# Kernel tuning notes

Hardware: AMD Instinct MI355X
Metric: run time of the kernel (lower is better)

The kernel has to match this reference:

```python
import jax, jax.numpy as jnp
import numpy as np

B, C, H, T, L = 128, 16, 9, 2048, 9  # batch, channels, sensors, time, decomp levels
TAU = 1.0

def _conv(x, w, pad):
    # x: [N,C,H,W], w: [O,I,kh,kw]
    return jax.lax.conv_general_dilated(x, w, (1, 1), pad,
                                        dimension_numbers=('NCHW', 'OIHW', 'NCHW'))

def _prelu(x, a):
    return jnp.where(x >= 0, x, a * x)

def _branch(z, w1, a, w2):
    # ReflectionPad2d((1,1,0,0)) -> Conv(1,3) -> PReLU -> Conv(1,1) -> Tanh
    z = jnp.pad(z, ((0, 0), (0, 0), (0, 0), (1, 1)), mode='reflect')
    z = _prelu(_conv(z, w1, [(0, 0), (0, 0)]), a)
    return jnp.tanh(_conv(z, w2, [(0, 0), (0, 0)]))


def setup_inputs() -> dict:
    key = jax.random.key(0)
    ks = jax.random.split(key, 24)
    n = lambda k, s, sc=0.05: jax.random.normal(k, s, dtype=jnp.float32) * sc
    u = jax.random.uniform(ks[1], (L, 2 * B, 2, 1, 1), dtype=jnp.float32,
                           minval=1e-6, maxval=1.0 - 1e-6)
    inp = {
        'x': jax.random.normal(ks[0], (B, 1, H, T), dtype=jnp.float32),
        'gumbel_noise': -jnp.log(-jnp.log(u)),
        # conv_in stem
        'Wc1': n(ks[2], (C, 1, 1, 33)), 'bc1': jnp.zeros((C,), jnp.float32),
        'bn1_g': jnp.ones((C,), jnp.float32), 'bn1_b': jnp.zeros((C,), jnp.float32),
        'a_c1': jnp.float32(0.25),
        'Wc2': n(ks[3], (C, C, 1, 3)), 'bc2': jnp.zeros((C,), jnp.float32),
        'bn2_g': jnp.ones((C,), jnp.float32), 'bn2_b': jnp.zeros((C,), jnp.float32),
        'a_c2': jnp.float32(0.25),
        # per-level lifting P/U branches
        'WP1': n(ks[4], (L, C, C, 1, 3)), 'aP': jnp.full((L,), 0.25, jnp.float32),
        'WP2': n(ks[5], (L, C, C, 1, 1)),
        'WU1': n(ks[6], (L, C, C, 1, 3)), 'aU': jnp.full((L,), 0.25, jnp.float32),
        'WU2': n(ks[7], (L, C, C, 1, 1)),
        # per-level gumble routing head (pooled -> 1x1 C->C -> PReLU -> 1x1 C->2 -> PReLU)
        'Wg1': n(ks[8], (L, C, C, 1, 1)), 'ag1': jnp.full((L,), 0.25, jnp.float32),
        'Wg2': n(ks[9], (L, 2, C, 1, 1)), 'ag2': jnp.full((L,), 0.25, jnp.float32),
    }
    return inp


def _forward(x, Wc1, bc1, bn1_g, bn1_b, a_c1, Wc2, bc2, bn2_g, bn2_b, a_c2,
             WP1, aP, WP2, WU1, aU, WU2, Wg1, ag1, Wg2, ag2, gumbel_noise):
    rs = lambda v: v.reshape(1, -1, 1, 1)
    # conv_in stem (BatchNorm in eval form with default running stats)
    x = _conv(x, Wc1, [(0, 0), (16, 16)]) + rs(bc1)
    x = _prelu(x * rs(bn1_g) + rs(bn1_b), a_c1)
    x = _conv(x, Wc2, [(0, 0), (1, 1)]) + rs(bc2)
    x = _prelu(x * rs(bn2_g) + rs(bn2_b), a_c2)  # [B,C,H,T]

    feats = []
    for i in range(L):
        even, odd = x[..., ::2], x[..., 1::2]
        # modified lifting: c = even + U(odd); d = odd - P(c)
        c = even + _branch(odd, WU1[i], aU[i], WU2[i])
        d = odd - _branch(c, WP1[i], aP[i], WP2[i])
        out = jnp.stack([c, d], axis=1)  # [B,2,C,H,t]
        t = out.shape[-1]
        # gumble_block_2D: pool each (low/high) slice to [2B,C,1,1]
        pooled = out.reshape(B * 2, C, H, t).mean(axis=(2, 3), keepdims=True)
        hm = _prelu(_conv(pooled, Wg1[i], [(0, 0), (0, 0)]), ag1[i])
        hm = _prelu(_conv(hm, Wg2[i], [(0, 0), (0, 0)]), ag2[i])  # [2B,2,1,1]
        s = jax.nn.softmax(hm, axis=1)
        m = jax.nn.softmax((s + gumbel_noise[i]) / TAU, axis=1)
        m = m.reshape(B, 2, 2, 1, 1)
        input_conv = out * m[:, :, 0][..., None]  # gated conv branch [B,2,C,H,t]
        input_res = out * m[:, :, 1][..., None]   # gated residual branch
        feats.append(input_res.mean(axis=-1))      # [B,2,C,H]
        x = input_conv[:, 0]                       # gated low-pass feeds next level
    return jnp.stack(feats, axis=-1)  # [B,2,C,H,L]


def reference(x, gumbel_noise, Wc1, bc1, bn1_g, bn1_b, a_c1, Wc2, bc2, bn2_g,
              bn2_b, a_c2, WP1, aP, WP2, WU1, aU, WU2, Wg1, ag1, Wg2, ag2):
    return _forward(x, Wc1, bc1, bn1_g, bn1_b, a_c1, Wc2, bc2, bn2_g, bn2_b,
                    a_c2, WP1, aP, WP2, WU1, aU, WU2, Wg1, ag1, Wg2, ag2,
                    gumbel_noise)
```

## Files before the change

kernel.cpp:

```cpp
#include <hip/hip_runtime.h>
#include <hip/hip_bf16.h>


#define CB 16
#define HH 9
#define TT0 2048
#define RS_SLOT 36864
#define LPITCH 20

__device__ __forceinline__ float ftanh(float x) {
    float e = __expf(2.f * x);
    return 1.f - 2.f / (e + 1.f);
}
__device__ __forceinline__ float fprelu(float v, float a) {
    return v >= 0.f ? v : a * v;
}
__device__ __forceinline__ void ld16(const float* p, float* v) {
#pragma unroll
    for (int q = 0; q < 4; ++q) {
        float4 f = *(const float4*)(p + 4 * q);
        v[4 * q] = f.x; v[4 * q + 1] = f.y; v[4 * q + 2] = f.z; v[4 * q + 3] = f.w;
    }
}
__device__ __forceinline__ void ld16s(const float* p, float* v) {
#pragma unroll
    for (int q = 0; q < 4; ++q) {
        float4 f = *(const float4*)(p + 4 * q);
        v[4 * q] = f.x; v[4 * q + 1] = f.y; v[4 * q + 2] = f.z; v[4 * q + 3] = f.w;
    }
}
__device__ __forceinline__ void st16(float* p, const float* v) {
#pragma unroll
    for (int q = 0; q < 4; ++q) {
        float4 f; f.x = v[4 * q]; f.y = v[4 * q + 1]; f.z = v[4 * q + 2]; f.w = v[4 * q + 3];
        *(float4*)(p + 4 * q) = f;
    }
}
__device__ __forceinline__ int refl(int u, int t) {
    return u < 0 ? -u : (u >= t ? 2 * t - 2 - u : u);
}

__device__ __forceinline__ void gate_eval(
    const float* __restrict__ g144, const float* __restrict__ Wg1,
    float ag1, float ag2, const float* __restrict__ Wg2,
    float inv, float gn0, float gn1, float* m0o, float* m1o)
{
    float pooled[CB];
#pragma unroll
    for (int cc = 0; cc < CB; ++cc) {
        float s = 0.f;
#pragma unroll
        for (int h = 0; h < HH; ++h) s += g144[cc * HH + h];
        pooled[cc] = s * inv;
    }
    float hm1[CB];
#pragma unroll
    for (int cc = 0; cc < CB; ++cc) {
        float s = 0.f;
#pragma unroll
        for (int c2 = 0; c2 < CB; ++c2) s = fmaf(Wg1[cc * CB + c2], pooled[c2], s);
        hm1[cc] = fprelu(s, ag1);
    }
    float h0 = 0.f, h1 = 0.f;
#pragma unroll
    for (int c2 = 0; c2 < CB; ++c2) {
        h0 = fmaf(Wg2[c2], hm1[c2], h0);
        h1 = fmaf(Wg2[CB + c2], hm1[c2], h1);
    }
    h0 = fprelu(h0, ag2); h1 = fprelu(h1, ag2);
    float mx = fmaxf(h0, h1);
    float e0 = __expf(h0 - mx), e1 = __expf(h1 - mx);
    float s0 = e0 / (e0 + e1), s1 = e1 / (e0 + e1);
    float a0 = s0 + gn0, a1 = s1 + gn1;
    float mx2 = fmaxf(a0, a1);
    float f0 = __expf(a0 - mx2), f1 = __expf(a1 - mx2);
    *m0o = f0 / (f0 + f1);
    *m1o = f1 / (f0 + f1);
}

__device__ __forceinline__ void rowsum_reduce(const float* vals, float* rs, int tile,
                                              int b, int h, int sdx, int tid) {
    __shared__ float red[4 * CB];
    const int lane = tid & 63, wv = tid >> 6;
    __syncthreads();
#pragma unroll
    for (int cc = 0; cc < CB; ++cc) {
        float s = vals[cc];
#pragma unroll
        for (int off = 32; off >= 1; off >>= 1) s += __shfl_xor(s, off, 64);
        if (lane == cc) red[wv * CB + cc] = s;
    }
    __syncthreads();
    if (tid < CB) {
        float s = red[tid] + red[CB + tid] + red[2 * CB + tid] + red[3 * CB + tid];
        rs[(size_t)tile * RS_SLOT + ((size_t)(2 * b + sdx) * CB + tid) * HH + h] = s;
    }
    __syncthreads();
}

__global__ void wtrans_kernel(const float* __restrict__ Wc1, const float* __restrict__ Wc2,
                              const float* __restrict__ WU1, const float* __restrict__ WU2,
                              const float* __restrict__ WP1, const float* __restrict__ WP2,
                              float* __restrict__ W)
{
    const int tid = threadIdx.x;
    for (int idx = tid; idx < 528; idx += 256) {
        int k = idx >> 4, cc = idx & 15;
        W[idx] = Wc1[cc * 33 + k];
    }
    for (int idx = tid; idx < 768; idx += 256) {
        int k = idx >> 8, c2 = (idx >> 4) & 15, cc = idx & 15;
        W[528 + idx] = Wc2[(cc * 16 + c2) * 3 + k];
    }
    for (int i = 0; i < 9; ++i) {
        float* base = W + 1296 + i * 2048;
        const float* wu1 = WU1 + i * 768;
        const float* wp1 = WP1 + i * 768;
        const float* wu2 = WU2 + i * 256;
        const float* wp2 = WP2 + i * 256;
        for (int idx = tid; idx < 768; idx += 256) {
            int k = idx >> 8, c2 = (idx >> 4) & 15, cc = idx & 15;
            base[idx]        = wu1[cc * 48 + c2 * 3 + k];
            base[1024 + idx] = wp1[cc * 48 + c2 * 3 + k];
        }
        if (tid < 256) {
            int c2 = tid >> 4, cc = tid & 15;
            base[768 + tid]  = wu2[cc * 16 + c2];
            base[1792 + tid] = wp2[cc * 16 + c2];
        }
    }
}

__device__ __forceinline__ void compute_c(
    const float* __restrict__ xrow, int j, int t, float sm,
    const float* __restrict__ W1, const float* __restrict__ W2, float aU,
    float* cv, float* ow1)
{
    float accz[CB];
#pragma unroll
    for (int i = 0; i < CB; ++i) accz[i] = 0.f;
#pragma unroll
    for (int k = 0; k < 3; ++k) {
        int um = refl(j - 1 + k, t);
        float ow[CB];
        ld16(xrow + (size_t)(2 * um + 1) * CB, ow);
        if (k == 1) {
#pragma unroll
            for (int i = 0; i < CB; ++i) ow1[i] = ow[i];
        }
#pragma unroll
        for (int c2 = 0; c2 < CB; ++c2) {
            float o = ow[c2];
            const float* wp = W1 + (k * 16 + c2) * 16;
#pragma unroll
            for (int cc = 0; cc < CB; ++cc)
                accz[cc] = fmaf(wp[cc], o, accz[cc]);
        }
    }
#pragma unroll
    for (int i = 0; i < CB; ++i) accz[i] = fprelu(accz[i], aU);
    float bacc[CB];
#pragma unroll
    for (int cc = 0; cc < CB; ++cc) bacc[cc] = 0.f;
#pragma unroll
    for (int c2 = 0; c2 < CB; ++c2) {
        float z = accz[c2];
        const float* wp = W2 + c2 * 16;
#pragma unroll
        for (int cc = 0; cc < CB; ++cc)
            bacc[cc] = fmaf(wp[cc], z, bacc[cc]);
    }
    float ev[CB];
    ld16(xrow + (size_t)(2 * j) * CB, ev);
#pragma unroll
    for (int cc = 0; cc < CB; ++cc)
        cv[cc] = sm * ev[cc] + ftanh(sm * bacc[cc]);
}

__device__ __forceinline__ void compute_d_tanh(
    const float* __restrict__ ldc_base, int j, int t, int seg0,
    const float* __restrict__ W1, const float* __restrict__ W2, float aP,
    float* tv)
{
    float accz[CB];
#pragma unroll
    for (int i = 0; i < CB; ++i) accz[i] = 0.f;
#pragma unroll
    for (int k = 0; k < 3; ++k) {
        int um = refl(j - 1 + k, t);
        float cw[CB];
        ld16s(ldc_base + (seg0 + um) * LPITCH, cw);
#pragma unroll
        for (int c2 = 0; c2 < CB; ++c2) {
            float o = cw[c2];
            const float* wp = W1 + (k * 16 + c2) * 16;
#pragma unroll
            for (int cc = 0; cc < CB; ++cc)
                accz[cc] = fmaf(wp[cc], o, accz[cc]);
        }
    }
#pragma unroll
    for (int i = 0; i < CB; ++i) accz[i] = fprelu(accz[i], aP);
    float bacc[CB];
#pragma unroll
    for (int cc = 0; cc < CB; ++cc) bacc[cc] = 0.f;
#pragma unroll
    for (int c2 = 0; c2 < CB; ++c2) {
        float z = accz[c2];
        const float* wp = W2 + c2 * 16;
#pragma unroll
        for (int cc = 0; cc < CB; ++cc)
            bacc[cc] = fmaf(wp[cc], z, bacc[cc]);
    }
#pragma unroll
    for (int cc = 0; cc < CB; ++cc) tv[cc] = ftanh(bacc[cc]);
}

__global__ __launch_bounds__(256, 4) void front_kernel(
    const float* __restrict__ x, const float* __restrict__ Wt,
    const float* __restrict__ bc1,
    const float* __restrict__ bn1g, const float* __restrict__ bn1b,
    const float* __restrict__ ac1,
    const float* __restrict__ bc2,
    const float* __restrict__ bn2g, const float* __restrict__ bn2b,
    const float* __restrict__ ac2,
    float* __restrict__ y)
{
    const int tid = threadIdx.x;
    const int t0  = blockIdx.x * 254;
    const int h   = blockIdx.y;
    const int b   = blockIdx.z;
    const float* Wc1t = Wt;
    const float* Wc2t = Wt + 528;

    __shared__ float lds_x[288];
    __shared__ float lds_y[256 * LPITCH];

    const float* xrow = x + (size_t)(b * HH + h) * TT0;
    {
        int g = t0 - 17 + tid;
        lds_x[tid] = (g >= 0 && g < TT0) ? xrow[g] : 0.f;
        if (tid < 32) {
            int g2 = t0 + 239 + tid;
            lds_x[256 + tid] = (g2 >= 0 && g2 < TT0) ? xrow[g2] : 0.f;
        }
    }
    __syncthreads();

    const float a1 = ac1[0], a2 = ac2[0];
    float acc[CB];
#pragma unroll
    for (int cc = 0; cc < CB; ++cc) acc[cc] = bc1[cc];
#pragma unroll
    for (int k = 0; k < 33; ++k) {
        float xv = lds_x[tid + k];
        const float* wp = Wc1t + k * 16;
#pragma unroll
        for (int cc = 0; cc < CB; ++cc) acc[cc] = fmaf(wp[cc], xv, acc[cc]);
    }
#pragma unroll
    for (int cc = 0; cc < CB; ++cc)
        lds_y[tid * LPITCH + cc] = fprelu(acc[cc] * bn1g[cc] + bn1b[cc], a1);
    __syncthreads();

    const int jt = t0 + tid;
    if (tid < 254 && jt < TT0) {
        float acc2[CB];
#pragma unroll
        for (int cc = 0; cc < CB; ++cc) acc2[cc] = bc2[cc];
#pragma unroll
        for (int k = 0; k < 3; ++k) {
            int u = jt - 1 + k;
            if (u >= 0 && u < TT0) {
                float yv[CB];
                ld16s(&lds_y[(tid + k) * LPITCH], yv);
#pragma unroll
                for (int c2 = 0; c2 < CB; ++c2) {
                    float yvv = yv[c2];
                    const float* wp = Wc2t + (k * 16 + c2) * 16;
#pragma unroll
                    for (int cc = 0; cc < CB; ++cc)
                        acc2[cc] = fmaf(wp[cc], yvv, acc2[cc]);
                }
            }
        }
        float ov[CB];
#pragma unroll
        for (int cc = 0; cc < CB; ++cc) ov[cc] = fprelu(acc2[cc] * bn2g[cc] + bn2b[cc], a2);
        st16(y + ((size_t)(b * HH + h) * TT0 + jt) * CB, ov);
    }
}

__global__ __launch_bounds__(256, 2) void cd_kernel(
    const float* __restrict__ xin, float* __restrict__ xout,
    float* __restrict__ rs_out, const float* __restrict__ rs_prev,
    const float* __restrict__ Wt,
    const float* __restrict__ aUp, const float* __restrict__ aPp,
    const float* __restrict__ gnp, const float* __restrict__ Wg1p,
    const float* __restrict__ ag1p, const float* __restrict__ Wg2p,
    const float* __restrict__ ag2p,
    float* __restrict__ out, const int t, const int nt_prev, const int li_prev)
{
    const int tid  = threadIdx.x;
    const int row  = blockIdx.x;
    const int tile = blockIdx.y;
    const int b = row / 9, h = row - 9 * b;
    const float aU = aUp[0], aP = aPp[0];
    const float* xrow = xin + (size_t)row * (2 * t) * CB;
    const int p0 = tile * 256;
    const int j = p0 + tid;
    const bool valid = (j < t);

    const float* WU1t = Wt;
    const float* WU2t = Wt + 768;
    const float* WP1t = Wt + 1024;
    const float* WP2t = Wt + 1792;

    __shared__ float ldc[258 * LPITCH];
    __shared__ float gsum[288];
    __shared__ float shv[3];

    float sm = 1.f;
    if (rs_prev) {
        const bool writer = (h == 0 && tile == 0);
        const int nload = writer ? 288 : 144;
        for (int idx = tid; idx < nload; idx += 256) {
            float s = 0.f;
            for (int sl = 0; sl < nt_prev; ++sl)
                s += rs_prev[(size_t)sl * RS_SLOT + (size_t)b * 288 + idx];
            gsum[idx] = s;
        }
        __syncthreads();
        if (tid == 0 || (writer && tid == 1)) {
            const float tp = 2.f * (float)t;
            float m0, m1;
            gate_eval(&gsum[tid * 144], Wg1p, ag1p[0], ag2p[0], Wg2p,
                      1.f / (9.f * tp), gnp[(2 * b + tid) * 2 + 0],
                      gnp[(2 * b + tid) * 2 + 1], &m0, &m1);
            if (tid == 0) { shv[0] = m0; shv[1] = m1 / tp; }
            else          { shv[2] = m1 / tp; }
        }
        __syncthreads();
        sm = shv[0];
        if (writer) {
            float sc0 = shv[1], sc1 = shv[2];
            for (int idx = tid; idx < 288; idx += 256)
                out[(size_t)((size_t)b * 288 + idx) * 9 + li_prev] =
                    gsum[idx] * (idx < 144 ? sc0 : sc1);
        }
    }

    float cv[CB], ow1[CB];
#pragma unroll
    for (int i = 0; i < CB; ++i) { cv[i] = 0.f; ow1[i] = 0.f; }

    if (valid) {
        compute_c(xrow, j, t, sm, WU1t, WU2t, aU, cv, ow1);
        st16(&ldc[(tid + 1) * LPITCH], cv);
        st16(xout + ((size_t)row * t + j) * CB, cv);
    }
    if (tid < 2) {
        int jx = (tid == 0) ? p0 - 1 : p0 + 256;
        if (jx >= 0 && jx < t) {
            float hv[CB], dump[CB];
            compute_c(xrow, jx, t, sm, WU1t, WU2t, aU, hv, dump);
            st16(&ldc[(jx - p0 + 1) * LPITCH], hv);
        }
    }

    rowsum_reduce(cv, rs_out, tile, b, h, 0, tid);

    float dv[CB];
#pragma unroll
    for (int i = 0; i < CB; ++i) dv[i] = 0.f;

    if (valid) {
        float tv[CB];
        compute_d_tanh(ldc, j, t, 1 - p0, WP1t, WP2t, aP, tv);
#pragma unroll
        for (int cc = 0; cc < CB; ++cc) dv[cc] = sm * ow1[cc] - tv[cc];
    }
    rowsum_reduce(dv, rs_out, tile, b, h, 1, tid);
}

__global__ __launch_bounds__(256, 2) void cd_small_kernel(
    const float* __restrict__ xin, float* __restrict__ xout,
    float* __restrict__ rs_out, const float* __restrict__ rs_prev,
    const float* __restrict__ Wt,
    const float* __restrict__ aUp, const float* __restrict__ aPp,
    const float* __restrict__ gnp, const float* __restrict__ Wg1p,
    const float* __restrict__ ag1p, const float* __restrict__ Wg2p,
    const float* __restrict__ ag2p,
    float* __restrict__ out, const int t, const int log2t, const int li_prev)
{
    const int tid  = threadIdx.x;
    const int j    = tid & (t - 1);
    const int rloc = tid >> log2t;
    const int row  = (blockIdx.x << (8 - log2t)) + rloc;
    const int b = row / 9, h = row - 9 * b;
    const float aU = aUp[0], aP = aPp[0];

    const float* gp = rs_prev + (size_t)b * 288;
    const float tp = 2.f * (float)t;
    float m0, m1;
    gate_eval(gp, Wg1p, ag1p[0], ag2p[0], Wg2p, 1.f / (9.f * tp),
              gnp[(2 * b) * 2 + 0], gnp[(2 * b) * 2 + 1], &m0, &m1);
    const float sm = m0;
    if (h == 0) {
        float m0x, m1x;
        gate_eval(gp + 144, Wg1p, ag1p[0], ag2p[0], Wg2p, 1.f / (9.f * tp),
                  gnp[(2 * b + 1) * 2 + 0], gnp[(2 * b + 1) * 2 + 1], &m0x, &m1x);
        float sc0 = m1 / tp, sc1 = m1x / tp;
        for (int idx = j; idx < 288; idx += t)
            out[(size_t)((size_t)b * 288 + idx) * 9 + li_prev] =
                gp[idx] * (idx < 144 ? sc0 : sc1);
    }

    const float* xrow = xin + (size_t)row * (2 * t) * CB;
    const float* WU1t = Wt;
    const float* WU2t = Wt + 768;
    const float* WP1t = Wt + 1024;
    const float* WP2t = Wt + 1792;

    __shared__ float ldc[256 * LPITCH];

    float cv[CB], ow1[CB];
    compute_c(xrow, j, t, sm, WU1t, WU2t, aU, cv, ow1);
    st16(&ldc[tid * LPITCH], cv);
    st16(xout + ((size_t)row * t + j) * CB, cv);
    __syncthreads();

    float tv[CB];
    compute_d_tanh(ldc, j, t, rloc << log2t, WP1t, WP2t, aP, tv);
    float dv[CB];
#pragma unroll
    for (int cc = 0; cc < CB; ++cc) dv[cc] = sm * ow1[cc] - tv[cc];

#pragma unroll
    for (int cc = 0; cc < CB; ++cc) {
        float s = cv[cc];
        for (int off = t >> 1; off >= 1; off >>= 1) s += __shfl_xor(s, off, 64);
        cv[cc] = s;
        float s2 = dv[cc];
        for (int off = t >> 1; off >= 1; off >>= 1) s2 += __shfl_xor(s2, off, 64);
        dv[cc] = s2;
    }
    if (j == 0) {
#pragma unroll
        for (int cc = 0; cc < CB; ++cc) {
            rs_out[((size_t)(2 * b + 0) * CB + cc) * HH + h] = cv[cc];
            rs_out[((size_t)(2 * b + 1) * CB + cc) * HH + h] = dv[cc];
        }
    }
}

__global__ __launch_bounds__(192) void gate_kernel(
    const float* __restrict__ rs, const float* __restrict__ gn,
    const float* __restrict__ Wg1, const float* __restrict__ ag1p,
    const float* __restrict__ Wg2, const float* __restrict__ ag2p,
    float* __restrict__ out, float* __restrict__ m0buf,
    const int t, const int nt, const int li)
{
    const int bj  = blockIdx.x;
    const int tid = threadIdx.x;

    __shared__ float sums[144];
    __shared__ float sscale;

    if (tid < 144) {
        float s = 0.f;
        for (int tl = 0; tl < nt; ++tl)
            s += rs[(size_t)tl * RS_SLOT + (size_t)bj * 144 + tid];
        sums[tid] = s;
    }
    __syncthreads();

    if (tid == 0) {
        float m0, m1;
        gate_eval(sums, Wg1, ag1p[0], ag2p[0], Wg2, 1.f / (9.f * (float)t),
                  gn[bj * 2 + 0], gn[bj * 2 + 1], &m0, &m1);
        sscale = m1 / (float)t;
        if ((bj & 1) == 0) m0buf[bj >> 1] = m0;
    }
    __syncthreads();

    if (tid < 144)
        out[(size_t)(bj * 144 + tid) * 9 + li] = sums[tid] * sscale;
}

extern "C" void kernel_launch(void* const* d_in, const int* in_sizes, int n_in,
                              void* d_out, int out_size, void* d_ws, size_t ws_size,
                              hipStream_t stream) {
    const float* x    = (const float*)d_in[0];
    const float* gn   = (const float*)d_in[1];
    const float* Wc1  = (const float*)d_in[2];
    const float* bc1  = (const float*)d_in[3];
    const float* bn1g = (const float*)d_in[4];
    const float* bn1b = (const float*)d_in[5];
    const float* ac1  = (const float*)d_in[6];
    const float* Wc2  = (const float*)d_in[7];
    const float* bc2  = (const float*)d_in[8];
    const float* bn2g = (const float*)d_in[9];
    const float* bn2b = (const float*)d_in[10];
    const float* ac2  = (const float*)d_in[11];
    const float* WP1  = (const float*)d_in[12];
    const float* aP   = (const float*)d_in[13];
    const float* WP2  = (const float*)d_in[14];
    const float* WU1  = (const float*)d_in[15];
    const float* aU   = (const float*)d_in[16];
    const float* WU2  = (const float*)d_in[17];
    const float* Wg1  = (const float*)d_in[18];
    const float* ag1  = (const float*)d_in[19];
    const float* Wg2  = (const float*)d_in[20];
    const float* ag2  = (const float*)d_in[21];
    float* out = (float*)d_out;

    char* ws = (char*)d_ws;
    const size_t sz0  = (size_t)128 * 9 * 2048 * 16 * 4;
    const size_t sz1  = sz0 / 2;
    const size_t rsz  = (size_t)4 * RS_SLOT * 4;
    float* buf0 = (float*)ws;
    float* buf1 = (float*)(ws + sz0);
    float* rsA  = (float*)(ws + sz0 + sz1);
    float* rsB  = (float*)(ws + sz0 + sz1 + rsz);
    float* m0s  = (float*)(ws + sz0 + sz1 + 2 * rsz);
    float* wt   = (float*)(ws + sz0 + sz1 + 2 * rsz + 512);

    wtrans_kernel<<<1, 256, 0, stream>>>(Wc1, Wc2, WU1, WU2, WP1, WP2, wt);

    dim3 fgrid(9, 9, 128);
    front_kernel<<<fgrid, 256, 0, stream>>>(x, wt, bc1, bn1g, bn1b, ac1,
                                            bc2, bn2g, bn2b, ac2, buf0);

    float* rsbuf[2] = {rsA, rsB};
    float* cur = buf0;
    float* nxt = buf1;
    int t = 1024;
    for (int i = 0; i < 9; ++i) {
        float* rs_out = rsbuf[i & 1];
        const float* rs_prev = (i == 0) ? nullptr : rsbuf[(i - 1) & 1];
        const float* lw   = wt + 1296 + i * 2048;
        const int ip      = (i >= 1) ? i - 1 : 0;
        const float* gnp  = gn  + ip * 512;
        const float* Wg1p = Wg1 + ip * 256;
        const float* Wg2p = Wg2 + ip * 32;
        const int nt_prev = (i >= 1) ? ((8 >> i) > 0 ? (8 >> i) : 1) : 0;
        if (t >= 128) {
            dim3 lgrid(128 * 9, (t > 256) ? (t >> 8) : 1);
            cd_kernel<<<lgrid, 256, 0, stream>>>(
                cur, nxt, rs_out, rs_prev, lw, aU + i, aP + i,
                gnp, Wg1p, ag1 + ip, Wg2p, ag2 + ip, out, t, nt_prev, ip);
        } else {
            int log2t = 31 - __builtin_clz(t);
            int nblk  = (1152 * t) >> 8;
            cd_small_kernel<<<nblk, 256, 0, stream>>>(
                cur, nxt, rs_out, rs_prev, lw, aU + i, aP + i,
                gnp, Wg1p, ag1 + ip, Wg2p, ag2 + ip, out, t, log2t, ip);
        }
        float* tmp = cur; cur = nxt; nxt = tmp;
        t >>= 1;
    }
    gate_kernel<<<256, 192, 0, stream>>>(
        rsbuf[0], gn + 8 * 512, Wg1 + 8 * 256, ag1 + 8, Wg2 + 8 * 32, ag2 + 8,
        out, m0s, 4, 1, 8);
}
```

Baseline: 816.7 us.

## Use packed v2f FMA and overlapping halo tiles in the lifting kernel

Rewrites the inner 16-channel FMA loops in the stem and lifting convolutions to use 2-wide vector FMA on float2 pairs, so the compiler can emit packed FP32 instructions. Separately, cd_kernel now tiles time in overlapping 254-wide tiles where every thread computes one c value including the halo. This removes the serial two-thread halo recomputation step, at the cost of more tiles per row and redundant halo work. The row-sum workspace grows from 4 to 6 slots per buffer to hold the extra tiles.

New measurement: 891.2 us. +9.1%, slower.

```diff
diff --git a/kernel.cpp b/kernel.cpp
--- a/kernel.cpp
+++ b/kernel.cpp
@@ -8,6 +8,8 @@
 #define RS_SLOT 36864
 #define LPITCH 20
 
+typedef float v2f __attribute__((ext_vector_type(2)));
+
 __device__ __forceinline__ float ftanh(float x) {
     float e = __expf(2.f * x);
     return 1.f - 2.f / (e + 1.f);
@@ -22,13 +24,6 @@
         v[4 * q] = f.x; v[4 * q + 1] = f.y; v[4 * q + 2] = f.z; v[4 * q + 3] = f.w;
     }
 }
-__device__ __forceinline__ void ld16s(const float* p, float* v) {
-#pragma unroll
-    for (int q = 0; q < 4; ++q) {
-        float4 f = *(const float4*)(p + 4 * q);
-        v[4 * q] = f.x; v[4 * q + 1] = f.y; v[4 * q + 2] = f.z; v[4 * q + 3] = f.w;
-    }
-}
 __device__ __forceinline__ void st16(float* p, const float* v) {
 #pragma unroll
     for (int q = 0; q < 4; ++q) {
@@ -38,6 +33,14 @@
 }
 __device__ __forceinline__ int refl(int u, int t) {
     return u < 0 ? -u : (u >= t ? 2 * t - 2 - u : u);
+}
+
+__device__ __forceinline__ void fma16(v2f* acc2, const float* __restrict__ Wrow, float o) {
+    const v2f* w2 = (const v2f*)Wrow;
+    v2f ob; ob.x = o; ob.y = o;
+#pragma unroll
+    for (int i = 0; i < 8; ++i)
+        acc2[i] = __builtin_elementwise_fma(w2[i], ob, acc2[i]);
 }
 
 __device__ __forceinline__ void gate_eval(
@@ -136,9 +139,9 @@
     const float* __restrict__ W1, const float* __restrict__ W2, float aU,
     float* cv, float* ow1)
 {
-    float accz[CB];
-#pragma unroll
-    for (int i = 0; i < CB; ++i) accz[i] = 0.f;
+    v2f accz[8];
+#pragma unroll
+    for (int i = 0; i < 8; ++i) { accz[i].x = 0.f; accz[i].y = 0.f; }
 #pragma unroll
     for (int k = 0; k < 3; ++k) {
         int um = refl(j - 1 + k, t);
@@ -149,32 +152,28 @@
             for (int i = 0; i < CB; ++i) ow1[i] = ow[i];
         }
 #pragma unroll
-        for (int c2 = 0; c2 < CB; ++c2) {
-            float o = ow[c2];
-            const float* wp = W1 + (k * 16 + c2) * 16;
-#pragma unroll
-            for (int cc = 0; cc < CB; ++cc)
-                accz[cc] = fmaf(wp[cc], o, accz[cc]);
-        }
-    }
-#pragma unroll
-    for (int i = 0; i < CB; ++i) accz[i] = fprelu(accz[i], aU);
-    float bacc[CB];
-#pragma unroll
-    for (int cc = 0; cc < CB; ++cc) bacc[cc] = 0.f;
-#pragma unroll
-    for (int c2 = 0; c2 < CB; ++c2) {
-        float z = accz[c2];
-        const float* wp = W2 + c2 * 16;
-#pragma unroll
-        for (int cc = 0; cc < CB; ++cc)
-            bacc[cc] = fmaf(wp[cc], z, bacc[cc]);
-    }
+        for (int c2 = 0; c2 < CB; ++c2)
+            fma16(accz, W1 + (k * 16 + c2) * 16, ow[c2]);
+    }
+    float z[CB];
+#pragma unroll
+    for (int i = 0; i < 8; ++i) {
+        z[2 * i]     = fprelu(accz[i].x, aU);
+        z[2 * i + 1] = fprelu(accz[i].y, aU);
+    }
+    v2f bacc[8];
+#pragma unroll
+    for (int i = 0; i < 8; ++i) { bacc[i].x = 0.f; bacc[i].y = 0.f; }
+#pragma unroll
+    for (int c2 = 0; c2 < CB; ++c2)
+        fma16(bacc, W2 + c2 * 16, z[c2]);
     float ev[CB];
     ld16(xrow + (size_t)(2 * j) * CB, ev);
 #pragma unroll
-    for (int cc = 0; cc < CB; ++cc)
-        cv[cc] = sm * ev[cc] + ftanh(sm * bacc[cc]);
+    for (int i = 0; i < 8; ++i) {
+        cv[2 * i]     = sm * ev[2 * i]     + ftanh(sm * bacc[i].x);
+        cv[2 * i + 1] = sm * ev[2 * i + 1] + ftanh(sm * bacc[i].y);
+    }
 }
 
 __device__ __forceinline__ void compute_d_tanh(
@@ -182,38 +181,35 @@
     const float* __restrict__ W1, const float* __restrict__ W2, float aP,
     float* tv)
 {
-    float accz[CB];
-#pragma unroll
-    for (int i = 0; i < CB; ++i) accz[i] = 0.f;
+    v2f accz[8];
+#pragma unroll
+    for (int i = 0; i < 8; ++i) { accz[i].x = 0.f; accz[i].y = 0.f; }
 #pragma unroll
     for (int k = 0; k < 3; ++k) {
         int um = refl(j - 1 + k, t);
         float cw[CB];
-        ld16s(ldc_base + (seg0 + um) * LPITCH, cw);
-#pragma unroll
-        for (int c2 = 0; c2 < CB; ++c2) {
-            float o = cw[c2];
-            const float* wp = W1 + (k * 16 + c2) * 16;
-#pragma unroll
-            for (int cc = 0; cc < CB; ++cc)
-                accz[cc] = fmaf(wp[cc], o, accz[cc]);
-        }
-    }
-#pragma unroll
-    for (int i = 0; i < CB; ++i) accz[i] = fprelu(accz[i], aP);
-    float bacc[CB];
-#pragma unroll
-    for (int cc = 0; cc < CB; ++cc) bacc[cc] = 0.f;
-#pragma unroll
-    for (int c2 = 0; c2 < CB; ++c2) {
-        float z = accz[c2];
-        const float* wp = W2 + c2 * 16;
-#pragma unroll
-        for (int cc = 0; cc < CB; ++cc)
-            bacc[cc] = fmaf(wp[cc], z, bacc[cc]);
-    }
-#pragma unroll
-    for (int cc = 0; cc < CB; ++cc) tv[cc] = ftanh(bacc[cc]);
+        ld16(ldc_base + (seg0 + um) * LPITCH, cw);
+#pragma unroll
+        for (int c2 = 0; c2 < CB; ++c2)
+            fma16(accz, W1 + (k * 16 + c2) * 16, cw[c2]);
+    }
+    float z[CB];
+#pragma unroll
+    for (int i = 0; i < 8; ++i) {
+        z[2 * i]     = fprelu(accz[i].x, aP);
+        z[2 * i + 1] = fprelu(accz[i].y, aP);
+    }
+    v2f bacc[8];
+#pragma unroll
+    for (int i = 0; i < 8; ++i) { bacc[i].x = 0.f; bacc[i].y = 0.f; }
+#pragma unroll
+    for (int c2 = 0; c2 < CB; ++c2)
+        fma16(bacc, W2 + c2 * 16, z[c2]);
+#pragma unroll
+    for (int i = 0; i < 8; ++i) {
+        tv[2 * i]     = ftanh(bacc[i].x);
+        tv[2 * i + 1] = ftanh(bacc[i].y);
+    }
 }
 
 __global__ __launch_bounds__(256, 4) void front_kernel(
@@ -248,45 +244,41 @@
     __syncthreads();
 
     const float a1 = ac1[0], a2 = ac2[0];
-    float acc[CB];
-#pragma unroll
-    for (int cc = 0; cc < CB; ++cc) acc[cc] = bc1[cc];
-#pragma unroll
-    for (int k = 0; k < 33; ++k) {
-        float xv = lds_x[tid + k];
-        const float* wp = Wc1t + k * 16;
-#pragma unroll
-        for (int cc = 0; cc < CB; ++cc) acc[cc] = fmaf(wp[cc], xv, acc[cc]);
-    }
-#pragma unroll
-    for (int cc = 0; cc < CB; ++cc)
-        lds_y[tid * LPITCH + cc] = fprelu(acc[cc] * bn1g[cc] + bn1b[cc], a1);
+    v2f acc[8];
+#pragma unroll
+    for (int i = 0; i < 8; ++i) { acc[i].x = bc1[2 * i]; acc[i].y = bc1[2 * i + 1]; }
+#pragma unroll
+    for (int k = 0; k < 33; ++k)
+        fma16(acc, Wc1t + k * 16, lds_x[tid + k]);
+#pragma unroll
+    for (int i = 0; i < 8; ++i) {
+        lds_y[tid * LPITCH + 2 * i]     = fprelu(acc[i].x * bn1g[2 * i] + bn1b[2 * i], a1);
+        lds_y[tid * LPITCH + 2 * i + 1] = fprelu(acc[i].y * bn1g[2 * i + 1] + bn1b[2 * i + 1], a1);
+    }
     __syncthreads();
 
     const int jt = t0 + tid;
     if (tid < 254 && jt < TT0) {
-        float acc2[CB];
-#pragma unroll
-        for (int cc = 0; cc < CB; ++cc) acc2[cc] = bc2[cc];
+        v2f acc2[8];
+#pragma unroll
+        for (int i = 0; i < 8; ++i) { acc2[i].x = bc2[2 * i]; acc2[i].y = bc2[2 * i + 1]; }
 #pragma unroll
         for (int k = 0; k < 3; ++k) {
             int u = jt - 1 + k;
             if (u >= 0 && u < TT0) {
                 float yv[CB];
-                ld16s(&lds_y[(tid + k) * LPITCH], yv);
-#pragma unroll
-                for (int c2 = 0; c2 < CB; ++c2) {
-                    float yvv = yv[c2];
-                    const float* wp = Wc2t + (k * 16 + c2) * 16;
-#pragma unroll
-                    for (int cc = 0; cc < CB; ++cc)
-                        acc2[cc] = fmaf(wp[cc], yvv, acc2[cc]);
-                }
+                ld16(&lds_y[(tid + k) * LPITCH], yv);
+#pragma unroll
+                for (int c2 = 0; c2 < CB; ++c2)
+                    fma16(acc2, Wc2t + (k * 16 + c2) * 16, yv[c2]);
             }
         }
         float ov[CB];
 #pragma unroll
-        for (int cc = 0; cc < CB; ++cc) ov[cc] = fprelu(acc2[cc] * bn2g[cc] + bn2b[cc], a2);
+        for (int i = 0; i < 8; ++i) {
+            ov[2 * i]     = fprelu(acc2[i].x * bn2g[2 * i] + bn2b[2 * i], a2);
+            ov[2 * i + 1] = fprelu(acc2[i].y * bn2g[2 * i + 1] + bn2b[2 * i + 1], a2);
+        }
         st16(y + ((size_t)(b * HH + h) * TT0 + jt) * CB, ov);
     }
 }
@@ -307,16 +299,17 @@
     const int b = row / 9, h = row - 9 * b;
     const float aU = aUp[0], aP = aPp[0];
     const float* xrow = xin + (size_t)row * (2 * t) * CB;
-    const int p0 = tile * 256;
-    const int j = p0 + tid;
-    const bool valid = (j < t);
+    const int q0 = tile * 254;
+    const int j = q0 - 1 + tid;
+    const bool cvalid = (j >= 0 && j < t);
+    const bool own = (tid >= 1 && tid <= 254 && j < t);
 
     const float* WU1t = Wt;
     const float* WU2t = Wt + 768;
     const float* WP1t = Wt + 1024;
     const float* WP2t = Wt + 1792;
 
-    __shared__ float ldc[258 * LPITCH];
+    __shared__ float ldc[256 * LPITCH];
     __shared__ float gsum[288];
     __shared__ float shv[3];
 
@@ -353,30 +346,29 @@
     float cv[CB], ow1[CB];
 #pragma unroll
     for (int i = 0; i < CB; ++i) { cv[i] = 0.f; ow1[i] = 0.f; }
-
-    if (valid) {
+    float sc[CB];
+#pragma unroll
+    for (int i = 0; i < CB; ++i) sc[i] = 0.f;
+
+    if (cvalid) {
         compute_c(xrow, j, t, sm, WU1t, WU2t, aU, cv, ow1);
-        st16(&ldc[(tid + 1) * LPITCH], cv);
-        st16(xout + ((size_t)row * t + j) * CB, cv);
-    }
-    if (tid < 2) {
-        int jx = (tid == 0) ? p0 - 1 : p0 + 256;
-        if (jx >= 0 && jx < t) {
-            float hv[CB], dump[CB];
-            compute_c(xrow, jx, t, sm, WU1t, WU2t, aU, hv, dump);
-            st16(&ldc[(jx - p0 + 1) * LPITCH], hv);
-        }
-    }
-
-    rowsum_reduce(cv, rs_out, tile, b, h, 0, tid);
+        st16(&ldc[tid * LPITCH], cv);
+        if (own) {
+            st16(xout + ((size_t)row * t + j) * CB, cv);
+#pragma unroll
+            for (int cc = 0; cc < CB; ++cc) sc[cc] = cv[cc];
+        }
+    }
+
+    rowsum_reduce(sc, rs_out, tile, b, h, 0, tid);
 
     float dv[CB];
 #pragma unroll
     for (int i = 0; i < CB; ++i) dv[i] = 0.f;
 
-    if (valid) {
+    if (own) {
         float tv[CB];
-        compute_d_tanh(ldc, j, t, 1 - p0, WP1t, WP2t, aP, tv);
+        compute_d_tanh(ldc, j, t, 1 - q0, WP1t, WP2t, aP, tv);
 #pragma unroll
         for (int cc = 0; cc < CB; ++cc) dv[cc] = sm * ow1[cc] - tv[cc];
     }
@@ -518,7 +510,7 @@
     char* ws = (char*)d_ws;
     const size_t sz0  = (size_t)128 * 9 * 2048 * 16 * 4;
     const size_t sz1  = sz0 / 2;
-    const size_t rsz  = (size_t)4 * RS_SLOT * 4;
+    const size_t rsz  = (size_t)6 * RS_SLOT * 4;
     float* buf0 = (float*)ws;
     float* buf1 = (float*)(ws + sz0);
     float* rsA  = (float*)(ws + sz0 + sz1);
@@ -544,9 +536,10 @@
         const float* gnp  = gn  + ip * 512;
         const float* Wg1p = Wg1 + ip * 256;
         const float* Wg2p = Wg2 + ip * 32;
-        const int nt_prev = (i >= 1) ? ((8 >> i) > 0 ? (8 >> i) : 1) : 0;
+        const int t_prev  = 2048 >> i;
+        const int nt_prev = (i >= 1) ? ((t_prev >= 128) ? (t_prev + 253) / 254 : 1) : 0;
         if (t >= 128) {
-            dim3 lgrid(128 * 9, (t > 256) ? (t >> 8) : 1);
+            dim3 lgrid(128 * 9, (t + 253) / 254);
             cd_kernel<<<lgrid, 256, 0, stream>>>(
                 cur, nxt, rs_out, rs_prev, lw, aU + i, aP + i,
                 gnp, Wg1p, ag1 + ip, Wg2p, ag2 + ip, out, t, nt_prev, ip);
```
